# Performance work log

Measured on AMD Instinct MI355X. Metric: run time of the kernel, lower is better.

Reference implementation:

```python
import jax, jax.numpy as jnp
import numpy as np

B, LQ, LK, D = 4, 256, 512, 256


def setup_inputs() -> dict:
    key = jax.random.key(0)
    k1, k2, k3, k4, k5, k6 = jax.random.split(key, 6)
    return {
        "query": jax.random.normal(k1, (B, LQ, D), dtype=jnp.float32),
        "key": jax.random.normal(k2, (B, LK, D), dtype=jnp.float32),
        "value": jax.random.normal(k3, (B, LK, D), dtype=jnp.float32),
        "W1": jax.random.normal(k4, (D, D), dtype=jnp.float32) * 0.06,
        "W2": jax.random.normal(k5, (D, D), dtype=jnp.float32) * 0.06,
        "v": jax.random.normal(k6, (D,), dtype=jnp.float32) * 0.06,
        "mask": jnp.ones((B, LQ, LK), dtype=jnp.int32),
    }


def reference(query, key, value, W1, W2, v, mask):
    # Linear layers are applied to the broadcast tensors in the original, but
    # they distribute over the add: W1(key) and W2(query) computed once each.
    hid_dim = query.shape[-1]
    scale = jnp.sqrt(jnp.asarray(hid_dim, dtype=query.dtype))
    W1_key = jnp.einsum("bkd,ed->bke", key, W1)     # [B, Lk, D]
    W2_query = jnp.einsum("bqd,ed->bqe", query, W2)  # [B, Lq, D]
    # tanh is nonlinear -> the [B, Lq, Lk, D] broadcast-add intermediate is
    # required by the math (this is the kernel-fusion opportunity).
    energy = jnp.tanh(W1_key[:, None, :, :] + W2_query[:, :, None, :])
    scores = jnp.einsum("bqkd,d->bqk", energy, v) / scale  # [B, Lq, Lk]
    scores = jnp.where(mask == 0, jnp.asarray(-1e10, scores.dtype), scores)
    attention = jax.nn.softmax(scores, axis=-1)
    context = jnp.einsum("bqk,bkd->bqd", attention, value)  # [B, Lq, D]
    return (context, attention)
```

## Files before the change

### kernel.cpp

```cpp
#include <hip/hip_runtime.h>
#include <math.h>

#define DD  256
#define LKK 512
#define LQQ 256
#define BB  4

constexpr float TWO_LOG2E = 2.8853900817779268f;
constexpr float LOG2E     = 1.4426950408889634f;
constexpr float CLAMPV    = 1e8f;

__device__ __forceinline__ float fast_rcp(float x)  { return __builtin_amdgcn_rcpf(x); }
__device__ __forceinline__ float fast_exp2(float x) { return __builtin_amdgcn_exp2f(x); }

#define COMP(v,u) ((u)==0?(v).x:(u)==1?(v).y:(u)==2?(v).z:(v).w)

__global__ __launch_bounds__(256) void gemm_expk2(const float* __restrict__ key,
                                                  const float* __restrict__ query,
                                                  const float* __restrict__ W1,
                                                  const float* __restrict__ W2,
                                                  float* __restrict__ EaT,
                                                  float* __restrict__ Eb) {
  __shared__ float Xs[16][36];
  __shared__ float Ws[16][68];
  const int tid = threadIdx.x;
  const bool isK = blockIdx.x < (BB * LKK / 32);
  const float* __restrict__ X = isK ? key : query;
  const float* __restrict__ W = isK ? W1 : W2;
  const int m0 = (isK ? blockIdx.x : blockIdx.x - BB * LKK / 32) * 32;
  const int e0 = blockIdx.y * 64;

  const int r0 = (tid >> 4) << 1;
  const int c0 = (tid & 15) << 2;
  const int xr = tid >> 3, xc = (tid & 7) << 1;
  const int wr = tid >> 2, wc = (tid & 3) << 2;

  float2 xv = *(const float2*)&X[(m0 + xr) * DD + xc];
  float4 wv = *(const float4*)&W[(e0 + wr) * DD + wc];

  float acc[2][4] = {};
  for (int k0 = 0; k0 < DD; k0 += 16) {
    __syncthreads();
    Xs[xc][xr] = xv.x; Xs[xc + 1][xr] = xv.y;
    Ws[wc][wr] = wv.x; Ws[wc + 1][wr] = wv.y; Ws[wc + 2][wr] = wv.z; Ws[wc + 3][wr] = wv.w;
    __syncthreads();
    if (k0 + 16 < DD) {
      xv = *(const float2*)&X[(m0 + xr) * DD + k0 + 16 + xc];
      wv = *(const float4*)&W[(e0 + wr) * DD + k0 + 16 + wc];
    }
#pragma unroll
    for (int k = 0; k < 16; ++k) {
      const float2 a  = *(const float2*)&Xs[k][r0];
      const float4 bq = *(const float4*)&Ws[k][c0];
      acc[0][0] = fmaf(a.x, bq.x, acc[0][0]); acc[0][1] = fmaf(a.x, bq.y, acc[0][1]);
      acc[0][2] = fmaf(a.x, bq.z, acc[0][2]); acc[0][3] = fmaf(a.x, bq.w, acc[0][3]);
      acc[1][0] = fmaf(a.y, bq.x, acc[1][0]); acc[1][1] = fmaf(a.y, bq.y, acc[1][1]);
      acc[1][2] = fmaf(a.y, bq.z, acc[1][2]); acc[1][3] = fmaf(a.y, bq.w, acc[1][3]);
    }
  }
  if (isK) {
    const int b = m0 >> 9;
    const int kloc = (m0 & 511) + r0;
#pragma unroll
    for (int j = 0; j < 4; ++j) {
      float2 o;
      o.x = fast_exp2(acc[0][j] * TWO_LOG2E);
      o.y = fast_exp2(acc[1][j] * TWO_LOG2E);
      *(float2*)&EaT[b * (DD * LKK) + (e0 + c0 + j) * LKK + kloc] = o;
    }
  } else {
#pragma unroll
    for (int i = 0; i < 2; ++i) {
      float4 o;
      o.x = fast_exp2(acc[i][0] * TWO_LOG2E);
      o.y = fast_exp2(acc[i][1] * TWO_LOG2E);
      o.z = fast_exp2(acc[i][2] * TWO_LOG2E);
      o.w = fast_exp2(acc[i][3] * TWO_LOG2E);
      *(float4*)&Eb[(m0 + r0 + i) * DD + e0 + c0] = o;
    }
  }
}

#define QUAD(CX, UB, ACC) do {                                        \
    const float A_  = fminf(fmaf(c0.CX, (UB).x, 1.f), CLAMPV);        \
    const float B_  = fminf(fmaf(c1.CX, (UB).y, 1.f), CLAMPV);        \
    const float C_  = fminf(fmaf(c2.CX, (UB).z, 1.f), CLAMPV);        \
    const float D_  = fminf(fmaf(c3.CX, (UB).w, 1.f), CLAMPV);        \
    const float AB_ = A_ * B_, CD_ = C_ * D_;                         \
    const float t1_ = fmaf(uvv.y, A_, uvv.x * B_);                    \
    const float t2_ = fmaf(uvv.w, C_, uvv.z * D_);                    \
    const float nm_ = fmaf(t1_, CD_, t2_ * AB_);                      \
    ACC = fmaf(nm_, fast_rcp(AB_ * CD_), ACC);                        \
  } while (0)

__global__ __launch_bounds__(512) void attn_fused(const float* __restrict__ EaT,
                                                  const float* __restrict__ Eb,
                                                  const float* __restrict__ vvec,
                                                  const float* __restrict__ value,
                                                  const int* __restrict__ mask,
                                                  float* __restrict__ ctx_out,
                                                  float* __restrict__ attn_out) {
  __shared__ float sc[4][LKK];
  __shared__ float part[4][LKK];
  __shared__ float scr[8][4][DD];

  const int tid = threadIdx.x;
  const int bid = blockIdx.x;
  const int b  = bid >> 6;
  const int q0 = (bid & 63) << 2;
  const int dh = tid >> 8;
  const int t  = tid & 255;
  const int k2 = t << 1;
  const int db = dh << 7;

  const float* __restrict__ eb0 = &Eb[(b * LQQ + q0) * DD];
  const float* __restrict__ eb1 = eb0 + DD;
  const float* __restrict__ eb2 = eb0 + 2 * DD;
  const float* __restrict__ eb3 = eb0 + 3 * DD;

  {
    const float* __restrict__ ea = &EaT[b * (DD * LKK) + db * LKK + k2];
    float a00 = 0.f, a10 = 0.f;
    float a01 = 0.f, a11 = 0.f;
    float a02 = 0.f, a12 = 0.f;
    float a03 = 0.f, a13 = 0.f;

    float2 c0 = *(const float2*)&ea[0 * LKK];
    float2 c1 = *(const float2*)&ea[1 * LKK];
    float2 c2 = *(const float2*)&ea[2 * LKK];
    float2 c3 = *(const float2*)&ea[3 * LKK];
    float4 ub0 = *(const float4*)&eb0[db];
    float4 ub1 = *(const float4*)&eb1[db];
    float4 ub2 = *(const float4*)&eb2[db];
    float4 ub3 = *(const float4*)&eb3[db];
    float4 uvv = *(const float4*)&vvec[db];

    for (int d = 0; d < 124; d += 4) {
      const float2 n0 = *(const float2*)&ea[(d + 4) * LKK];
      const float2 n1 = *(const float2*)&ea[(d + 5) * LKK];
      const float2 n2 = *(const float2*)&ea[(d + 6) * LKK];
      const float2 n3 = *(const float2*)&ea[(d + 7) * LKK];
      const float4 nb0 = *(const float4*)&eb0[db + d + 4];
      const float4 nb1 = *(const float4*)&eb1[db + d + 4];
      const float4 nb2 = *(const float4*)&eb2[db + d + 4];
      const float4 nb3 = *(const float4*)&eb3[db + d + 4];
      const float4 nvv = *(const float4*)&vvec[db + d + 4];
      QUAD(x, ub0, a00); QUAD(y, ub0, a10);
      QUAD(x, ub1, a01); QUAD(y, ub1, a11);
      QUAD(x, ub2, a02); QUAD(y, ub2, a12);
      QUAD(x, ub3, a03); QUAD(y, ub3, a13);
      c0 = n0; c1 = n1; c2 = n2; c3 = n3;
      ub0 = nb0; ub1 = nb1; ub2 = nb2; ub3 = nb3; uvv = nvv;
    }
    QUAD(x, ub0, a00); QUAD(y, ub0, a10);
    QUAD(x, ub1, a01); QUAD(y, ub1, a11);
    QUAD(x, ub2, a02); QUAD(y, ub2, a12);
    QUAD(x, ub3, a03); QUAD(y, ub3, a13);

    if (dh == 1) {
      *(float2*)&part[0][k2] = make_float2(a00, a10);
      *(float2*)&part[1][k2] = make_float2(a01, a11);
      *(float2*)&part[2][k2] = make_float2(a02, a12);
      *(float2*)&part[3][k2] = make_float2(a03, a13);
    }
    __syncthreads();
    if (dh == 0) {
      float Sv = 0.f;
#pragma unroll
      for (int d4 = 0; d4 < DD; d4 += 4) {
        const float4 vv = *(const float4*)&vvec[d4];
        Sv += (vv.x + vv.y) + (vv.z + vv.w);
      }
      const float inv_scale = 0.0625f;
      float accx[4] = {a00, a01, a02, a03};
      float accy[4] = {a10, a11, a12, a13};
#pragma unroll
      for (int q = 0; q < 4; ++q) {
        const float2 p = *(const float2*)&part[q][k2];
        float2 s;
        s.x = (Sv - 2.f * (accx[q] + p.x)) * inv_scale;
        s.y = (Sv - 2.f * (accy[q] + p.y)) * inv_scale;
        const int2 mq = *(const int2*)&mask[(b * LQQ + q0 + q) * LKK + k2];
        if (mq.x == 0) s.x = -1e10f;
        if (mq.y == 0) s.y = -1e10f;
        *(float2*)&sc[q][k2] = s;
      }
    }
  }
  __syncthreads();

  {
    const int w = tid >> 6, lane = tid & 63;
    if (w < 4) {
      float e_[8];
      float mx = -3.4e38f;
#pragma unroll
      for (int i = 0; i < 8; ++i) { e_[i] = sc[w][(i << 6) + lane]; mx = fmaxf(mx, e_[i]); }
#pragma unroll
      for (int off = 32; off; off >>= 1) mx = fmaxf(mx, __shfl_xor(mx, off));
      float sum = 0.f;
#pragma unroll
      for (int i = 0; i < 8; ++i) { e_[i] = fast_exp2((e_[i] - mx) * LOG2E); sum += e_[i]; }
#pragma unroll
      for (int off = 32; off; off >>= 1) sum += __shfl_xor(sum, off);
      const float inv = fast_rcp(sum);
      const int arow = (b * LQQ + q0 + w) * LKK;
#pragma unroll
      for (int i = 0; i < 8; ++i) {
        const float p = e_[i] * inv;
        attn_out[arow + (i << 6) + lane] = p;
        sc[w][(i << 6) + lane] = p;
      }
    }
  }
  __syncthreads();

  {
    const int kh = tid >> 6, dv = (tid & 63) << 2;
    const int kb = kh << 6;
    float4 c[4] = {};
    const float* __restrict__ vb = &value[(b * LKK + kb) * DD + dv];
    for (int s = 0; s < 64; s += 4) {
      const float4 p0v = *(const float4*)&sc[0][kb + s];
      const float4 p1v = *(const float4*)&sc[1][kb + s];
      const float4 p2v = *(const float4*)&sc[2][kb + s];
      const float4 p3v = *(const float4*)&sc[3][kb + s];
#pragma unroll
      for (int u = 0; u < 4; ++u) {
        const float4 vv = *(const float4*)vb; vb += DD;
        const float a0 = COMP(p0v, u), a1 = COMP(p1v, u);
        const float a2 = COMP(p2v, u), a3 = COMP(p3v, u);
        c[0].x = fmaf(a0, vv.x, c[0].x); c[0].y = fmaf(a0, vv.y, c[0].y);
        c[0].z = fmaf(a0, vv.z, c[0].z); c[0].w = fmaf(a0, vv.w, c[0].w);
        c[1].x = fmaf(a1, vv.x, c[1].x); c[1].y = fmaf(a1, vv.y, c[1].y);
        c[1].z = fmaf(a1, vv.z, c[1].z); c[1].w = fmaf(a1, vv.w, c[1].w);
        c[2].x = fmaf(a2, vv.x, c[2].x); c[2].y = fmaf(a2, vv.y, c[2].y);
        c[2].z = fmaf(a2, vv.z, c[2].z); c[2].w = fmaf(a2, vv.w, c[2].w);
        c[3].x = fmaf(a3, vv.x, c[3].x); c[3].y = fmaf(a3, vv.y, c[3].y);
        c[3].z = fmaf(a3, vv.z, c[3].z); c[3].w = fmaf(a3, vv.w, c[3].w);
      }
    }
#pragma unroll
    for (int q = 0; q < 4; ++q)
      *(float4*)&scr[kh][q][dv] = c[q];
  }
  __syncthreads();

  if (tid < 256) {
    const int qq = tid >> 6, d4 = (tid & 63) << 2;
    float4 s4 = make_float4(0.f, 0.f, 0.f, 0.f);
#pragma unroll
    for (int kh2 = 0; kh2 < 8; ++kh2) {
      const float4 rr = *(const float4*)&scr[kh2][qq][d4];
      s4.x += rr.x; s4.y += rr.y; s4.z += rr.z; s4.w += rr.w;
    }
    *(float4*)&ctx_out[(b * LQQ + q0 + qq) * DD + d4] = s4;
  }
}

extern "C" void kernel_launch(void* const* d_in, const int* in_sizes, int n_in,
                              void* d_out, int out_size, void* d_ws, size_t ws_size,
                              hipStream_t stream) {
  const float* query = (const float*)d_in[0];
  const float* key   = (const float*)d_in[1];
  const float* value = (const float*)d_in[2];
  const float* W1    = (const float*)d_in[3];
  const float* W2    = (const float*)d_in[4];
  const float* v     = (const float*)d_in[5];
  const int*   mask  = (const int*)d_in[6];

  float* out      = (float*)d_out;
  float* ctx_out  = out;
  float* attn_out = out + BB * LQQ * DD;

  float* EaT = (float*)d_ws;
  float* Eb  = EaT + BB * DD * LKK;

  dim3 g1(BB * LKK / 32 + BB * LQQ / 32, DD / 64);
  gemm_expk2<<<g1, 256, 0, stream>>>(key, query, W1, W2, EaT, Eb);

  attn_fused<<<256, 512, 0, stream>>>(EaT, Eb, v, value, mask, ctx_out, attn_out);
}
```

Baseline: 50.20 us.

## Widen score register tile to 4 keys and split D into four slices; deepen GEMM K-tile

In the fused attention kernel each thread now computes 4 keys by 4 queries instead of 2 keys by 4 queries, and the D reduction is split across four thread groups of 64 rather than two of 128. Partial sums from the other three groups go through a larger shared buffer. The aim is more reuse of each Eb/v load per key, with 4-wide vector loads of EaT. The projection GEMM also moves from a K-tile of 16 to 32, halving its barrier count. The costs are more LDS use and register pressure at 512 threads, and a three-way partial reduction done by only a quarter of the threads.

```diff
diff --git a/kernel.cpp b/kernel.cpp
--- a/kernel.cpp
+++ b/kernel.cpp
@@ -21,8 +21,8 @@
                                                   const float* __restrict__ W2,
                                                   float* __restrict__ EaT,
                                                   float* __restrict__ Eb) {
-  __shared__ float Xs[16][36];
-  __shared__ float Ws[16][68];
+  __shared__ float Xs[32][36];
+  __shared__ float Ws[32][68];
   const int tid = threadIdx.x;
   const bool isK = blockIdx.x < (BB * LKK / 32);
   const float* __restrict__ X = isK ? key : query;
@@ -32,24 +32,27 @@
 
   const int r0 = (tid >> 4) << 1;
   const int c0 = (tid & 15) << 2;
-  const int xr = tid >> 3, xc = (tid & 7) << 1;
-  const int wr = tid >> 2, wc = (tid & 3) << 2;
-
-  float2 xv = *(const float2*)&X[(m0 + xr) * DD + xc];
-  float4 wv = *(const float4*)&W[(e0 + wr) * DD + wc];
+  const int xr = tid >> 3, xc = (tid & 7) << 2;
+  const int wr = tid >> 2, wc = (tid & 3) << 3;
+
+  float4 xv  = *(const float4*)&X[(m0 + xr) * DD + xc];
+  float4 wv0 = *(const float4*)&W[(e0 + wr) * DD + wc];
+  float4 wv1 = *(const float4*)&W[(e0 + wr) * DD + wc + 4];
 
   float acc[2][4] = {};
-  for (int k0 = 0; k0 < DD; k0 += 16) {
+  for (int k0 = 0; k0 < DD; k0 += 32) {
     __syncthreads();
-    Xs[xc][xr] = xv.x; Xs[xc + 1][xr] = xv.y;
-    Ws[wc][wr] = wv.x; Ws[wc + 1][wr] = wv.y; Ws[wc + 2][wr] = wv.z; Ws[wc + 3][wr] = wv.w;
+    Xs[xc + 0][xr] = xv.x; Xs[xc + 1][xr] = xv.y; Xs[xc + 2][xr] = xv.z; Xs[xc + 3][xr] = xv.w;
+    Ws[wc + 0][wr] = wv0.x; Ws[wc + 1][wr] = wv0.y; Ws[wc + 2][wr] = wv0.z; Ws[wc + 3][wr] = wv0.w;
+    Ws[wc + 4][wr] = wv1.x; Ws[wc + 5][wr] = wv1.y; Ws[wc + 6][wr] = wv1.z; Ws[wc + 7][wr] = wv1.w;
     __syncthreads();
-    if (k0 + 16 < DD) {
-      xv = *(const float2*)&X[(m0 + xr) * DD + k0 + 16 + xc];
-      wv = *(const float4*)&W[(e0 + wr) * DD + k0 + 16 + wc];
-    }
-#pragma unroll
-    for (int k = 0; k < 16; ++k) {
+    if (k0 + 32 < DD) {
+      xv  = *(const float4*)&X[(m0 + xr) * DD + k0 + 32 + xc];
+      wv0 = *(const float4*)&W[(e0 + wr) * DD + k0 + 32 + wc];
+      wv1 = *(const float4*)&W[(e0 + wr) * DD + k0 + 32 + wc + 4];
+    }
+#pragma unroll
+    for (int k = 0; k < 32; ++k) {
       const float2 a  = *(const float2*)&Xs[k][r0];
       const float4 bq = *(const float4*)&Ws[k][c0];
       acc[0][0] = fmaf(a.x, bq.x, acc[0][0]); acc[0][1] = fmaf(a.x, bq.y, acc[0][1]);
@@ -81,7 +84,7 @@
   }
 }
 
-#define QUAD(CX, UB, ACC) do {                                        \
+#define QUAD4(CX, UB, ACC) do {                                       \
     const float A_  = fminf(fmaf(c0.CX, (UB).x, 1.f), CLAMPV);        \
     const float B_  = fminf(fmaf(c1.CX, (UB).y, 1.f), CLAMPV);        \
     const float C_  = fminf(fmaf(c2.CX, (UB).z, 1.f), CLAMPV);        \
@@ -101,17 +104,17 @@
                                                   float* __restrict__ ctx_out,
                                                   float* __restrict__ attn_out) {
   __shared__ float sc[4][LKK];
-  __shared__ float part[4][LKK];
+  __shared__ float part[12 * LKK];
   __shared__ float scr[8][4][DD];
 
   const int tid = threadIdx.x;
   const int bid = blockIdx.x;
   const int b  = bid >> 6;
   const int q0 = (bid & 63) << 2;
-  const int dh = tid >> 8;
-  const int t  = tid & 255;
-  const int k2 = t << 1;
-  const int db = dh << 7;
+  const int dh = tid >> 7;
+  const int t  = tid & 127;
+  const int k4 = t << 2;
+  const int db = dh << 6;
 
   const float* __restrict__ eb0 = &Eb[(b * LQQ + q0) * DD];
   const float* __restrict__ eb1 = eb0 + DD;
@@ -119,49 +122,45 @@
   const float* __restrict__ eb3 = eb0 + 3 * DD;
 
   {
-    const float* __restrict__ ea = &EaT[b * (DD * LKK) + db * LKK + k2];
-    float a00 = 0.f, a10 = 0.f;
-    float a01 = 0.f, a11 = 0.f;
-    float a02 = 0.f, a12 = 0.f;
-    float a03 = 0.f, a13 = 0.f;
-
-    float2 c0 = *(const float2*)&ea[0 * LKK];
-    float2 c1 = *(const float2*)&ea[1 * LKK];
-    float2 c2 = *(const float2*)&ea[2 * LKK];
-    float2 c3 = *(const float2*)&ea[3 * LKK];
+    const float* __restrict__ ea = &EaT[b * (DD * LKK) + db * LKK + k4];
+    float4 acc[4] = {};
+
+    float4 c0 = *(const float4*)&ea[0 * LKK];
+    float4 c1 = *(const float4*)&ea[1 * LKK];
+    float4 c2 = *(const float4*)&ea[2 * LKK];
+    float4 c3 = *(const float4*)&ea[3 * LKK];
     float4 ub0 = *(const float4*)&eb0[db];
     float4 ub1 = *(const float4*)&eb1[db];
     float4 ub2 = *(const float4*)&eb2[db];
     float4 ub3 = *(const float4*)&eb3[db];
     float4 uvv = *(const float4*)&vvec[db];
 
-    for (int d = 0; d < 124; d += 4) {
-      const float2 n0 = *(const float2*)&ea[(d + 4) * LKK];
-      const float2 n1 = *(const float2*)&ea[(d + 5) * LKK];
-      const float2 n2 = *(const float2*)&ea[(d + 6) * LKK];
-      const float2 n3 = *(const float2*)&ea[(d + 7) * LKK];
+    for (int d = 0; d < 60; d += 4) {
+      const float4 n0 = *(const float4*)&ea[(d + 4) * LKK];
+      const float4 n1 = *(const float4*)&ea[(d + 5) * LKK];
+      const float4 n2 = *(const float4*)&ea[(d + 6) * LKK];
+      const float4 n3 = *(const float4*)&ea[(d + 7) * LKK];
       const float4 nb0 = *(const float4*)&eb0[db + d + 4];
       const float4 nb1 = *(const float4*)&eb1[db + d + 4];
       const float4 nb2 = *(const float4*)&eb2[db + d + 4];
       const float4 nb3 = *(const float4*)&eb3[db + d + 4];
       const float4 nvv = *(const float4*)&vvec[db + d + 4];
-      QUAD(x, ub0, a00); QUAD(y, ub0, a10);
-      QUAD(x, ub1, a01); QUAD(y, ub1, a11);
-      QUAD(x, ub2, a02); QUAD(y, ub2, a12);
-      QUAD(x, ub3, a03); QUAD(y, ub3, a13);
+      QUAD4(x, ub0, acc[0].x); QUAD4(y, ub0, acc[0].y); QUAD4(z, ub0, acc[0].z); QUAD4(w, ub0, acc[0].w);
+      QUAD4(x, ub1, acc[1].x); QUAD4(y, ub1, acc[1].y); QUAD4(z, ub1, acc[1].z); QUAD4(w, ub1, acc[1].w);
+      QUAD4(x, ub2, acc[2].x); QUAD4(y, ub2, acc[2].y); QUAD4(z, ub2, acc[2].z); QUAD4(w, ub2, acc[2].w);
+      QUAD4(x, ub3, acc[3].x); QUAD4(y, ub3, acc[3].y); QUAD4(z, ub3, acc[3].z); QUAD4(w, ub3, acc[3].w);
       c0 = n0; c1 = n1; c2 = n2; c3 = n3;
       ub0 = nb0; ub1 = nb1; ub2 = nb2; ub3 = nb3; uvv = nvv;
     }
-    QUAD(x, ub0, a00); QUAD(y, ub0, a10);
-    QUAD(x, ub1, a01); QUAD(y, ub1, a11);
-    QUAD(x, ub2, a02); QUAD(y, ub2, a12);
-    QUAD(x, ub3, a03); QUAD(y, ub3, a13);
-
-    if (dh == 1) {
-      *(float2*)&part[0][k2] = make_float2(a00, a10);
-      *(float2*)&part[1][k2] = make_float2(a01, a11);
-      *(float2*)&part[2][k2] = make_float2(a02, a12);
-      *(float2*)&part[3][k2] = make_float2(a03, a13);
+    QUAD4(x, ub0, acc[0].x); QUAD4(y, ub0, acc[0].y); QUAD4(z, ub0, acc[0].z); QUAD4(w, ub0, acc[0].w);
+    QUAD4(x, ub1, acc[1].x); QUAD4(y, ub1, acc[1].y); QUAD4(z, ub1, acc[1].z); QUAD4(w, ub1, acc[1].w);
+    QUAD4(x, ub2, acc[2].x); QUAD4(y, ub2, acc[2].y); QUAD4(z, ub2, acc[2].z); QUAD4(w, ub2, acc[2].w);
+    QUAD4(x, ub3, acc[3].x); QUAD4(y, ub3, acc[3].y); QUAD4(z, ub3, acc[3].z); QUAD4(w, ub3, acc[3].w);
+
+    if (dh != 0) {
+#pragma unroll
+      for (int q = 0; q < 4; ++q)
+        *(float4*)&part[((dh - 1) * 4 + q) * LKK + k4] = acc[q];
     }
     __syncthreads();
     if (dh == 0) {
@@ -172,18 +171,22 @@
         Sv += (vv.x + vv.y) + (vv.z + vv.w);
       }
       const float inv_scale = 0.0625f;
-      float accx[4] = {a00, a01, a02, a03};
-      float accy[4] = {a10, a11, a12, a13};
 #pragma unroll
       for (int q = 0; q < 4; ++q) {
-        const float2 p = *(const float2*)&part[q][k2];
-        float2 s;
-        s.x = (Sv - 2.f * (accx[q] + p.x)) * inv_scale;
-        s.y = (Sv - 2.f * (accy[q] + p.y)) * inv_scale;
-        const int2 mq = *(const int2*)&mask[(b * LQQ + q0 + q) * LKK + k2];
+        const float4 p1 = *(const float4*)&part[(0 * 4 + q) * LKK + k4];
+        const float4 p2 = *(const float4*)&part[(1 * 4 + q) * LKK + k4];
+        const float4 p3 = *(const float4*)&part[(2 * 4 + q) * LKK + k4];
+        float4 s;
+        s.x = (Sv - 2.f * (acc[q].x + p1.x + p2.x + p3.x)) * inv_scale;
+        s.y = (Sv - 2.f * (acc[q].y + p1.y + p2.y + p3.y)) * inv_scale;
+        s.z = (Sv - 2.f * (acc[q].z + p1.z + p2.z + p3.z)) * inv_scale;
+        s.w = (Sv - 2.f * (acc[q].w + p1.w + p2.w + p3.w)) * inv_scale;
+        const int4 mq = *(const int4*)&mask[(b * LQQ + q0 + q) * LKK + k4];
         if (mq.x == 0) s.x = -1e10f;
         if (mq.y == 0) s.y = -1e10f;
-        *(float2*)&sc[q][k2] = s;
+        if (mq.z == 0) s.z = -1e10f;
+        if (mq.w == 0) s.w = -1e10f;
+        *(float4*)&sc[q][k4] = s;
       }
     }
   }
```

Result: faster. 46.42 us (-7.5%).
